# Performance work log

Hardware: AMD Instinct MI355X
Metric: run time of the kernel (lower is better)

Reference implementation:

```python
import jax, jax.numpy as jnp
import numpy as np
from jax import lax

NEG = -1e30  # safe stand-in for -inf in float32
BLANK = 0


def _ctc_loss(log_probs, targets, logits_lengths, targets_lengths):
    # log_probs: (B, T, V) log-softmax over V; targets: (B, S) with labels in [1, V)
    B, T, V = log_probs.shape
    S = targets.shape[1]
    L = 2 * S + 1

    # extended target sequence with interleaved blanks: [b, t0, b, t1, ..., b]
    ext = jnp.full((B, L), BLANK, dtype=targets.dtype)
    ext = ext.at[:, 1::2].set(targets)

    # skip transition (s-2 -> s) allowed iff ext[s] != blank and ext[s] != ext[s-2]
    shifted2 = jnp.concatenate([jnp.full((B, 2), -1, dtype=ext.dtype), ext[:, :-2]], axis=1)
    skip = (ext != BLANK) & (ext != shifted2)  # (B, L)

    # gather per-time log-probs of extended labels: (B, T, L) -> scan axis first (T, B, L)
    lp_ext = jnp.take_along_axis(log_probs, ext[:, None, :], axis=2)
    xs = jnp.moveaxis(lp_ext, 1, 0)

    alpha0 = jnp.where(jnp.arange(L) == 0, 0.0, NEG).astype(log_probs.dtype)
    alpha0 = jnp.broadcast_to(alpha0, (B, L))

    def step(alpha, inputs):
        lp_t, t = inputs
        a2 = jnp.pad(alpha[:, :-1], ((0, 0), (1, 0)), constant_values=NEG)
        a3 = jnp.pad(alpha[:, :-2], ((0, 0), (2, 0)), constant_values=NEG)
        a3 = jnp.where(skip, a3, NEG)
        new = jnp.logaddexp(jnp.logaddexp(alpha, a2), a3) + lp_t
        # freeze alpha past each sequence's length
        alpha = jnp.where((t < logits_lengths)[:, None], new, alpha)
        return alpha, None

    alpha, _ = lax.scan(step, alpha0, (xs, jnp.arange(T)))

    # final states: last label (2*len-1) and trailing blank (2*len)
    e1 = (2 * targets_lengths - 1)[:, None]
    e2 = (2 * targets_lengths)[:, None]
    l1 = jnp.take_along_axis(alpha, e1, axis=1)[:, 0]
    l2 = jnp.take_along_axis(alpha, e2, axis=1)[:, 0]
    return -jnp.logaddexp(l1, l2)  # (B,)


def setup_inputs() -> dict:
    key = jax.random.key(0)
    k1, k2, k3, k4 = jax.random.split(key, 4)
    B, T, V, S = 64, 2000, 256, 200
    logits = jax.random.normal(k1, (B, T, V), dtype=jnp.float32)
    targets = jax.random.randint(k2, (B, S), 1, V)  # avoid blank=0
    logits_lengths = jax.random.randint(k3, (B,), 1500, T + 1)
    targets_lengths = jax.random.randint(k4, (B,), 150, S + 1)
    return {"logits": logits, "targets": targets,
            "logits_lengths": logits_lengths, "targets_lengths": targets_lengths}


def reference(logits, targets, logits_lengths, targets_lengths):
    # after_logsoftmax=False, time_major=False, reduce=None -> per-sample loss (B,)
    log_probs = jax.nn.log_softmax(logits, axis=2)
    return _ctc_loss(log_probs, targets, logits_lengths, targets_lengths)
```

## Files before the change

### kernel.cpp

```cpp
#include <hip/hip_runtime.h>
#include <hip/hip_bf16.h>
#include <cstdint>

#define NEG  (-1e30f)
#define VSZ  256
#define TCAP 2048
#define LN2F 0.6931471805599453f

static __device__ __forceinline__ float    uifu(unsigned u) { return __uint_as_float(u); }
static __device__ __forceinline__ unsigned f2bf(float f) {
    unsigned u = __float_as_uint(f);
    return (u + 0x7fffu + ((u >> 16) & 1u)) >> 16;
}

static __device__ __forceinline__ unsigned pkbf(float lo, float hi) {
    unsigned r;
    asm("v_cvt_pk_bf16_f32 %0, %1, %2" : "=v"(r) : "v"(lo), "v"(hi));
    return r;
}

static __device__ __forceinline__ float wave_sum_dpp(float v) {
    v += __int_as_float(__builtin_amdgcn_update_dpp(0, __float_as_int(v), 0x111, 0xf, 0xf, true));
    v += __int_as_float(__builtin_amdgcn_update_dpp(0, __float_as_int(v), 0x112, 0xf, 0xf, true));
    v += __int_as_float(__builtin_amdgcn_update_dpp(0, __float_as_int(v), 0x114, 0xf, 0xf, true));
    v += __int_as_float(__builtin_amdgcn_update_dpp(0, __float_as_int(v), 0x118, 0xf, 0xf, true));
    v += __int_as_float(__builtin_amdgcn_update_dpp(0, __float_as_int(v), 0x142, 0xa, 0xf, true));
    v += __int_as_float(__builtin_amdgcn_update_dpp(0, __float_as_int(v), 0x143, 0xc, 0xf, true));
    return __int_as_float(__builtin_amdgcn_readlane(__float_as_int(v), 63));
}

__global__ __launch_bounds__(256) void prep7(const float* __restrict__ logits,
                                             const int* __restrict__ targets,
                                             unsigned short* __restrict__ po,
                                             float* __restrict__ pbf,
                                             int T, int S) {
    const int b    = blockIdx.y;
    const int lane = threadIdx.x & 63;
    const int wv   = threadIdx.x >> 6;
    const int rt   = blockIdx.x * 4 + wv;
    if (rt >= T) return;
    const size_t row = (size_t)b * T + rt;
    __shared__ float ldse[4][VSZ];

    const float4* p = (const float4*)(logits + row * VSZ);
    float4 x = p[lane];
    float4 e;
    e.x = __expf(x.x); e.y = __expf(x.y); e.z = __expf(x.z); e.w = __expf(x.w);
    ((float4*)&ldse[wv][0])[lane] = e;

    float s  = (e.x + e.y) + (e.z + e.w);
    float tot = wave_sum_dpp(s);
    float rs  = __builtin_amdgcn_rcpf(tot);

    const int* tg = targets + (size_t)b * S;
    const int c0 = 4 * lane;
    uint2 st;
    if ((S & 3) == 0) {
        int4 tgv = *(const int4*)(tg + min(c0, S - 4));
        float g0 = ldse[wv][tgv.x] * rs;
        float g1 = ldse[wv][tgv.y] * rs;
        float g2 = ldse[wv][tgv.z] * rs;
        float g3 = ldse[wv][tgv.w] * rs;
        st.x = pkbf(g0, g1);
        st.y = pkbf(g2, g3);
    } else {
        float g0 = 0.f, g1 = 0.f, g2 = 0.f, g3 = 0.f;
        if (c0     < S) g0 = ldse[wv][tg[c0]]     * rs;
        if (c0 + 1 < S) g1 = ldse[wv][tg[c0 + 1]] * rs;
        if (c0 + 2 < S) g2 = ldse[wv][tg[c0 + 2]] * rs;
        if (c0 + 3 < S) g3 = ldse[wv][tg[c0 + 3]] * rs;
        st.x = pkbf(g0, g1);
        st.y = pkbf(g2, g3);
    }
    ((uint2*)(po + row * VSZ))[lane] = st;
    if (lane == 0) pbf[row] = e.x * rs;
}

typedef __attribute__((address_space(1))) unsigned int g1u_t;
typedef __attribute__((address_space(3))) unsigned int l3u_t;

static __device__ __forceinline__ void dma16(const void* g, void* l) {
    __builtin_amdgcn_global_load_lds((g1u_t*)(uintptr_t)g,
                                     (l3u_t*)(unsigned int)(uintptr_t)l, 16, 0, 0);
}
static __device__ __forceinline__ void dma4(const void* g, void* l) {
    __builtin_amdgcn_global_load_lds((g1u_t*)(uintptr_t)g,
                                     (l3u_t*)(unsigned int)(uintptr_t)l, 4, 0, 0);
}
static __device__ __forceinline__ float dpp_shr1_f(float v) {
    return __int_as_float(__builtin_amdgcn_update_dpp(0, __float_as_int(v), 0x138, 0xf, 0xf, true));
}
static __device__ __forceinline__ float dpp_shl1_f(float v) {
    return __int_as_float(__builtin_amdgcn_update_dpp(0, __float_as_int(v), 0x130, 0xf, 0xf, true));
}
static __device__ __forceinline__ int dpp_shr1_i(int v) {
    return __builtin_amdgcn_update_dpp(0, v, 0x138, 0xf, 0xf, true);
}
static __device__ __forceinline__ int dpp_shl1_i(int v) {
    return __builtin_amdgcn_update_dpp(0, v, 0x130, 0xf, 0xf, true);
}

template<int W>
static __device__ __forceinline__ void scan_dir(const unsigned short* __restrict__ po_b,
                                                const float* __restrict__ pbr,
                                                unsigned short* __restrict__ d0,
                                                unsigned short* __restrict__ d1,
                                                float* __restrict__ p0,
                                                float* __restrict__ p1,
                                                int lenD, int lm1, int i,
                                                float m1, float m3, float m5, float m7, float n7,
                                                float A[8], int& E) {
    const int  lhalf = i & 31;
    const bool hi    = (i >= 32);
    float dscale = 1.f;

    uint2 ra0, ra1, ra2, ra3, ra4, ra5, ra6, ra7;
    uint2 rb0, rb1, rb2, rb3, rb4, rb5, rb6, rb7;
    float4 qaA, qaB, qbA, qbB;

#define ROWOF(t_) (W ? max(lm1 - (t_), 0) : min((t_), lm1))

#define BODY(XV, PBV) { \
    float pA = uifu(XV.x << 16); \
    float pB = uifu(XV.x & 0xffff0000u); \
    float pC = uifu(XV.y << 16); \
    float pD = uifu(XV.y & 0xffff0000u); \
    if (W == 0) { \
        float hs = dpp_shr1_f(A[7]) * dscale; \
        float s7 = fmaf(m7, A[5], A[6]) + A[7]; \
        float s5 = fmaf(m5, A[3], A[4]) + A[5]; \
        float s3 = fmaf(m3, A[1], A[2]) + A[3]; \
        float s1 = fmaf(m1, hs,   A[0]) + A[1]; \
        A[7] = s7 * pD;  A[6] = (A[6] + A[5]) * (PBV); \
        A[5] = s5 * pC;  A[4] = (A[4] + A[3]) * (PBV); \
        A[3] = s3 * pB;  A[2] = (A[2] + A[1]) * (PBV); \
        A[1] = s1 * pA;  A[0] = (A[0] + hs)   * (PBV); \
    } else { \
        float q0 = A[0] * (PBV), q1 = A[1] * pA; \
        float q2 = A[2] * (PBV), q3 = A[3] * pB; \
        float q4 = A[4] * (PBV), q5 = A[5] * pC; \
        float q6 = A[6] * (PBV), q7 = A[7] * pD; \
        float nq0 = dpp_shl1_f(q0) * dscale; \
        float nq1 = dpp_shl1_f(q1) * dscale; \
        A[0] = q0 + q1; \
        A[1] = fmaf(m3, q3, q1 + q2); \
        A[2] = q2 + q3; \
        A[3] = fmaf(m5, q5, q3 + q4); \
        A[4] = q4 + q5; \
        A[5] = fmaf(m7, q7, q5 + q6); \
        A[6] = q6 + q7; \
        A[7] = fmaf(n7, nq1, q7 + nq0); \
    } \
}

#define RENORM { \
    float lmx = fmaxf(fmaxf(fmaxf(A[0], A[1]), fmaxf(A[2], A[3])), \
                      fmaxf(fmaxf(A[4], A[5]), fmaxf(A[6], A[7]))); \
    unsigned mb = __float_as_uint(lmx) >> 23; \
    mb = mb > 253u ? 253u : mb; \
    float sc_ = uifu((254u - mb) << 23); \
    A[0] *= sc_; A[1] *= sc_; A[2] *= sc_; A[3] *= sc_; \
    A[4] *= sc_; A[5] *= sc_; A[6] *= sc_; A[7] *= sc_; \
    E += (int)mb - 127; \
    int he = W ? dpp_shl1_i(E) : dpp_shr1_i(E); \
    int d  = min(max(he - E, -100), 100); \
    dscale = uifu((unsigned)(d + 127) << 23); \
}

#define STAGE(DN, PN_, TBASE) { \
    _Pragma("unroll") \
    for (int u = 0; u < 32; u += 2) { \
        const int rA = ROWOF((TBASE) + u), rB = ROWOF((TBASE) + u + 1); \
        dma16(po_b + (size_t)(hi ? rB : rA) * VSZ + 8 * lhalf, (DN) + (size_t)u * VSZ); \
    } \
    dma4(pbr + ROWOF((TBASE) + lhalf), (PN_)); \
}

#define LDB(R, QA, QB, DC, PC, BASE) { \
    R##0 = *(const uint2*)((DC) + (size_t)((BASE) + 0) * VSZ + 4 * i); \
    R##1 = *(const uint2*)((DC) + (size_t)((BASE) + 1) * VSZ + 4 * i); \
    R##2 = *(const uint2*)((DC) + (size_t)((BASE) + 2) * VSZ + 4 * i); \
    R##3 = *(const uint2*)((DC) + (size_t)((BASE) + 3) * VSZ + 4 * i); \
    R##4 = *(const uint2*)((DC) + (size_t)((BASE) + 4) * VSZ + 4 * i); \
    R##5 = *(const uint2*)((DC) + (size_t)((BASE) + 5) * VSZ + 4 * i); \
    R##6 = *(const uint2*)((DC) + (size_t)((BASE) + 6) * VSZ + 4 * i); \
    R##7 = *(const uint2*)((DC) + (size_t)((BASE) + 7) * VSZ + 4 * i); \
    QA = *(const float4*)((PC) + (BASE)); \
    QB = *(const float4*)((PC) + (BASE) + 4); \
}

#define CMP8(R, QA, QB) { \
    BODY(R##0, QA.x) BODY(R##1, QA.y) BODY(R##2, QA.z) BODY(R##3, QA.w) RENORM \
    BODY(R##4, QB.x) BODY(R##5, QB.y) BODY(R##6, QB.z) BODY(R##7, QB.w) RENORM \
}

#define SBAR __builtin_amdgcn_sched_barrier(0)

#define SUPERF(DC, PC, DN, PN_) { \
    STAGE(DN, PN_, t0 + 32) \
    asm volatile("s_waitcnt vmcnt(17)" ::: "memory"); \
    LDB(ra, qaA, qaB, DC, PC, 0) \
    SBAR; \
    LDB(rb, qbA, qbB, DC, PC, 8) \
    SBAR; \
    CMP8(ra, qaA, qaB) \
    LDB(ra, qaA, qaB, DC, PC, 16) \
    SBAR; \
    CMP8(rb, qbA, qbB) \
    LDB(rb, qbA, qbB, DC, PC, 24) \
    SBAR; \
    CMP8(ra, qaA, qaB) \
    CMP8(rb, qbA, qbB) \
}

    STAGE(d0, p0, 0)

    int t0 = 0;
    const int nfull = lenD >> 5;
    const int ntail = lenD & 31;
    unsigned short* cur = d0; unsigned short* nxt = d1;
    float* pc = p0;  float* pn = p1;

    #pragma clang loop unroll(disable)
    for (int sl = 0; sl < nfull; ++sl) {
        SUPERF(cur, pc, nxt, pn)
        t0 += 32;
        unsigned short* td = cur; cur = nxt; nxt = td;
        float* tp = pc; pc = pn; pn = tp;
    }
    if (ntail) {
        asm volatile("s_waitcnt vmcnt(0)" ::: "memory");
        #pragma clang loop unroll(disable)
        for (int u = 0; u < ntail; ++u) {
            uint2 x = *(const uint2*)(cur + (size_t)u * VSZ + 4 * i);
            float pb = pc[u];
            BODY(x, pb)
            if ((u & 3) == 3) RENORM
        }
    }
#undef SUPERF
#undef SBAR
#undef CMP8
#undef LDB
#undef STAGE
#undef RENORM
#undef BODY
#undef ROWOF
}

__global__ __launch_bounds__(128, 1) void ctc_scan12(const unsigned short* __restrict__ po,
                                                     const float* __restrict__ pbf,
                                                     const int* __restrict__ targets,
                                                     const int* __restrict__ llen_p,
                                                     const int* __restrict__ tlen_p,
                                                     float* __restrict__ out,
                                                     int T, int S) {
    const int b   = blockIdx.x;
    const int w   = threadIdx.x >> 6;
    const int i   = threadIdx.x & 63;
    const int len  = llen_p[b];
    const int lm1  = len - 1;
    const int lenF = (len + 1) >> 1;
    const int lenD = w ? (len - lenF) : lenF;

    __shared__ __align__(16) unsigned short dF0[32 * VSZ], dF1[32 * VSZ];
    __shared__ __align__(16) unsigned short dB0[32 * VSZ], dB1[32 * VSZ];
    __shared__ __align__(16) float pF0[64], pF1[64], pB0[64], pB1[64];
    __shared__ __align__(16) float bfin[512];
    __shared__ int bein[64];

    const int* tg  = targets + (size_t)b * S;
    const int Sm1  = S - 1;
    const int j0   = 4 * i;
    const int tm   = tg[max(min(j0 - 1, Sm1), 0)];
    const int t0l  = tg[min(j0,     Sm1)];
    const int t1l  = tg[min(j0 + 1, Sm1)];
    const int t2l  = tg[min(j0 + 2, Sm1)];
    const int t3l  = tg[min(j0 + 3, Sm1)];
    const int t4l  = tg[min(j0 + 4, Sm1)];
    const float m1 = (j0 == 0 || t0l != tm) ? 1.f : 0.f;
    const float m3 = (t1l != t0l) ? 1.f : 0.f;
    const float m5 = (t2l != t1l) ? 1.f : 0.f;
    const float m7 = (t3l != t2l) ? 1.f : 0.f;
    const float n7 = (t4l != t3l) ? 1.f : 0.f;

    const unsigned short* po_b = po + (size_t)b * T * VSZ;
    const float*          pbr  = pbf + (size_t)b * T;

    float A[8];
    int   E = 0;
    if (w == 0) {
        #pragma unroll
        for (int k = 0; k < 8; ++k) A[k] = 0.f;
        if (i == 0) A[0] = 1.f;
        scan_dir<0>(po_b, pbr, dF0, dF1, pF0, pF1,
                    lenD, lm1, i, m1, m3, m5, m7, n7, A, E);
    } else {
        const int tl = tlen_p[b];
        const int s1 = 2 * tl - 1, s2 = 2 * tl;
        #pragma unroll
        for (int k = 0; k < 8; ++k)
            A[k] = (8 * i + k == s1 || 8 * i + k == s2) ? 1.f : 0.f;
        scan_dir<1>(po_b, pbr, dB0, dB1, pB0, pB1,
                    lenD, lm1, i, m1, m3, m5, m7, n7, A, E);
        *(float4*)&bfin[8 * i]     = make_float4(A[0], A[1], A[2], A[3]);
        *(float4*)&bfin[8 * i + 4] = make_float4(A[4], A[5], A[6], A[7]);
        bein[i] = E;
    }
    __syncthreads();
    if (w == 0) {
        float4 u0 = *(float4*)&bfin[8 * i];
        float4 u1 = *(float4*)&bfin[8 * i + 4];
        float dsum = A[0]*u0.x + A[1]*u0.y + A[2]*u0.z + A[3]*u0.w
                   + A[4]*u1.x + A[5]*u1.y + A[6]*u1.z + A[7]*u1.w;
        float li = (dsum > 0.f) ? __logf(dsum) + (float)(E + bein[i]) * LN2F : NEG;
        float mx = li;
        #pragma unroll
        for (int off = 32; off; off >>= 1) mx = fmaxf(mx, __shfl_xor(mx, off, 64));
        float ss = __expf(li - mx);
        #pragma unroll
        for (int off = 32; off; off >>= 1) ss += __shfl_xor(ss, off, 64);
        if (i == 0) out[b] = -(mx + __logf(ss));
    }
}

__device__ __forceinline__ void barrier_lgkm() {
    __asm__ volatile("s_waitcnt lgkmcnt(0)\n\ts_barrier" ::: "memory");
}

__global__ __launch_bounds__(256) void lse_kernel(const float* __restrict__ logits,
                                                  float* __restrict__ lse,
                                                  int nrows) {
    int row = blockIdx.x * 4 + (threadIdx.x >> 6);
    if (row >= nrows) return;
    int lane = threadIdx.x & 63;
    const float4* p = (const float4*)(logits + (size_t)row * VSZ);
    float4 x = p[lane];
    float m = fmaxf(fmaxf(x.x, x.y), fmaxf(x.z, x.w));
    #pragma unroll
    for (int off = 32; off; off >>= 1) m = fmaxf(m, __shfl_xor(m, off, 64));
    float s = __expf(x.x - m) + __expf(x.y - m) + __expf(x.z - m) + __expf(x.w - m);
    #pragma unroll
    for (int off = 32; off; off >>= 1) s += __shfl_xor(s, off, 64);
    if (lane == 0) lse[row] = m + __logf(s);
}

__device__ __forceinline__ float lae(float a, float b) {
    float mx = fmaxf(a, b);
    float mn = fminf(a, b);
    return mx + __logf(1.0f + __expf(mn - mx));
}

__global__ __launch_bounds__(256, 1) void ctc_scan_fb(const float* __restrict__ logits,
                                                      const int* __restrict__ targets,
                                                      const int* __restrict__ llen_p,
                                                      const int* __restrict__ tlen_p,
                                                      const float* __restrict__ lse,
                                                      float* __restrict__ out,
                                                      int T, int S) {
    const int b = blockIdx.x;
    const int i = threadIdx.x;
    const int len = llen_p[b];

    __shared__ float blankv[TCAP];
    __shared__ float abuf[2][256 + 2];
    __shared__ float wsum[4];

    const float* __restrict__ lgb  = logits + (size_t)b * T * VSZ;
    const float* __restrict__ lseb = lse + (size_t)b * T;

    int  lab  = 0;
    bool skip = false;
    if (i < S) {
        lab = targets[b * S + i];
        int prev = (i >= 1) ? targets[b * S + i - 1] : -1;
        skip = (lab != prev);
    }
    for (int t = i; t < len; t += 256) blankv[t] = lgb[(size_t)t * VSZ];
    if (i < 2) abuf[i][0] = NEG;
    __syncthreads();

    float aEven = (i == 0) ? 0.0f : NEG;
    float aOdd  = NEG;
    const int lm1 = len - 1;
    float v0 = lgb[(size_t)lab];
    float v1 = lgb[(size_t)min(1, lm1) * VSZ + lab];
    float v2 = lgb[(size_t)min(2, lm1) * VSZ + lab];

    for (int t = 0; t < len; ++t) {
        float v3 = lgb[(size_t)min(t + 3, lm1) * VSZ + lab];
        float blv = blankv[t];
        abuf[t & 1][i + 1] = aOdd;
        barrier_lgkm();
        float nb = abuf[t & 1][i];
        float ne = lae(aEven, nb) + blv;
        float no = lae(lae(aOdd, aEven), skip ? nb : NEG) + v0;
        aEven = ne; aOdd = no;
        v0 = v1; v1 = v2; v2 = v3;
    }

    blankv[2 * i]     = aEven;
    blankv[2 * i + 1] = aOdd;
    float part = 0.f;
    for (int t = i; t < len; t += 256) part += lseb[t];
    #pragma unroll
    for (int off = 32; off; off >>= 1) part += __shfl_xor(part, off, 64);
    if ((i & 63) == 0) wsum[i >> 6] = part;
    __syncthreads();
    if (i == 0) {
        int tl = tlen_p[b];
        float s = wsum[0] + wsum[1] + wsum[2] + wsum[3];
        out[b] = s - lae(blankv[2 * tl - 1], blankv[2 * tl]);
    }
}

extern "C" void kernel_launch(void* const* d_in, const int* in_sizes, int n_in,
                              void* d_out, int out_size, void* d_ws, size_t ws_size,
                              hipStream_t stream) {
    const float* logits  = (const float*)d_in[0];
    const int*   targets = (const int*)d_in[1];
    const int*   llen    = (const int*)d_in[2];
    const int*   tlen    = (const int*)d_in[3];
    float*       out     = (float*)d_out;

    const int B = in_sizes[2];
    const int S = in_sizes[1] / B;
    const int T = in_sizes[0] / (B * VSZ);
    const int nrows = B * T;

    const size_t need = (size_t)nrows * VSZ * sizeof(unsigned short)
                      + (size_t)nrows * sizeof(float);
    if (ws_size >= need) {
        unsigned short* po = (unsigned short*)d_ws;
        float* pbf = (float*)(po + (size_t)nrows * VSZ);
        dim3 grid((T + 3) / 4, B);
        prep7<<<grid, 256, 0, stream>>>(logits, targets, po, pbf, T, S);
        ctc_scan12<<<B, 128, 0, stream>>>(po, pbf, targets, llen, tlen, out, T, S);
    } else {
        float* lse = (float*)d_ws;
        lse_kernel<<<(nrows + 3) / 4, 256, 0, stream>>>(logits, lse, nrows);
        ctc_scan_fb<<<B, 256, 0, stream>>>(logits, targets, llen, tlen, lse, out, T, S);
    }
}
```

Before: 263.6 us.

## Split global-to-LDS staging into dedicated producer waves with barrier handoff

```diff
diff --git a/kernel.cpp b/kernel.cpp
--- a/kernel.cpp
+++ b/kernel.cpp
@@ -100,25 +100,43 @@
     return __builtin_amdgcn_update_dpp(0, v, 0x130, 0xf, 0xf, true);
 }
 
+#define ROWOF(t_) (W ? max(lm1 - (t_), 0) : min((t_), lm1))
+
 template<int W>
-static __device__ __forceinline__ void scan_dir(const unsigned short* __restrict__ po_b,
-                                                const float* __restrict__ pbr,
-                                                unsigned short* __restrict__ d0,
-                                                unsigned short* __restrict__ d1,
-                                                float* __restrict__ p0,
-                                                float* __restrict__ p1,
-                                                int lenD, int lm1, int i,
-                                                float m1, float m3, float m5, float m7, float n7,
-                                                float A[8], int& E) {
+static __device__ __forceinline__ void stage_dir(const unsigned short* __restrict__ po_b,
+                                                 const float* __restrict__ pbr,
+                                                 unsigned short* __restrict__ d0,
+                                                 unsigned short* __restrict__ d1,
+                                                 float* __restrict__ p0,
+                                                 float* __restrict__ p1,
+                                                 int lenD, int lm1, int i, int nwinMax) {
     const int  lhalf = i & 31;
     const bool hi    = (i >= 32);
-    float dscale = 1.f;
-
-    uint2 ra0, ra1, ra2, ra3, ra4, ra5, ra6, ra7;
-    uint2 rb0, rb1, rb2, rb3, rb4, rb5, rb6, rb7;
-    float4 qaA, qaB, qbA, qbB;
-
-#define ROWOF(t_) (W ? max(lm1 - (t_), 0) : min((t_), lm1))
+    const int  nwin  = (lenD + 31) >> 5;
+
+#define STAGE(DN, PN_, TBASE) { \
+    _Pragma("unroll") \
+    for (int u = 0; u < 32; u += 2) { \
+        const int rA = ROWOF((TBASE) + u), rB = ROWOF((TBASE) + u + 1); \
+        dma16(po_b + (size_t)(hi ? rB : rA) * VSZ + 8 * lhalf, (DN) + (size_t)u * VSZ); \
+    } \
+    dma4(pbr + ROWOF((TBASE) + lhalf), (PN_)); \
+}
+
+    STAGE(d0, p0, 0)
+    asm volatile("s_waitcnt vmcnt(0)" ::: "memory");
+    #pragma clang loop unroll(disable)
+    for (int k = 0; k < nwinMax; ++k) {
+        __syncthreads();
+        if (k + 1 < nwin) {
+            unsigned short* DN = ((k + 1) & 1) ? d1 : d0;
+            float*          PN = ((k + 1) & 1) ? p1 : p0;
+            STAGE(DN, PN, 32 * (k + 1))
+            asm volatile("s_waitcnt vmcnt(0)" ::: "memory");
+        }
+    }
+#undef STAGE
+}
 
 #define BODY(XV, PBV) { \
     float pA = uifu(XV.x << 16); \
@@ -167,15 +185,6 @@
     dscale = uifu((unsigned)(d + 127) << 23); \
 }
 
-#define STAGE(DN, PN_, TBASE) { \
-    _Pragma("unroll") \
-    for (int u = 0; u < 32; u += 2) { \
-        const int rA = ROWOF((TBASE) + u), rB = ROWOF((TBASE) + u + 1); \
-        dma16(po_b + (size_t)(hi ? rB : rA) * VSZ + 8 * lhalf, (DN) + (size_t)u * VSZ); \
-    } \
-    dma4(pbr + ROWOF((TBASE) + lhalf), (PN_)); \
-}
-
 #define LDB(R, QA, QB, DC, PC, BASE) { \
     R##0 = *(const uint2*)((DC) + (size_t)((BASE) + 0) * VSZ + 4 * i); \
     R##1 = *(const uint2*)((DC) + (size_t)((BASE) + 1) * VSZ + 4 * i); \
@@ -196,59 +205,59 @@
 
 #define SBAR __builtin_amdgcn_sched_barrier(0)
 
-#define SUPERF(DC, PC, DN, PN_) { \
-    STAGE(DN, PN_, t0 + 32) \
-    asm volatile("s_waitcnt vmcnt(17)" ::: "memory"); \
-    LDB(ra, qaA, qaB, DC, PC, 0) \
-    SBAR; \
-    LDB(rb, qbA, qbB, DC, PC, 8) \
-    SBAR; \
-    CMP8(ra, qaA, qaB) \
-    LDB(ra, qaA, qaB, DC, PC, 16) \
-    SBAR; \
-    CMP8(rb, qbA, qbB) \
-    LDB(rb, qbA, qbB, DC, PC, 24) \
-    SBAR; \
-    CMP8(ra, qaA, qaB) \
-    CMP8(rb, qbA, qbB) \
-}
-
-    STAGE(d0, p0, 0)
-
-    int t0 = 0;
+template<int W>
+static __device__ __forceinline__ void scan_dir(const unsigned short* __restrict__ d0,
+                                                const unsigned short* __restrict__ d1,
+                                                const float* __restrict__ p0,
+                                                const float* __restrict__ p1,
+                                                int lenD, int i,
+                                                float m1, float m3, float m5, float m7, float n7,
+                                                float A[8], int& E, int nwinMax) {
+    float dscale = 1.f;
+    uint2 ra0, ra1, ra2, ra3, ra4, ra5, ra6, ra7;
+    uint2 rb0, rb1, rb2, rb3, rb4, rb5, rb6, rb7;
+    float4 qaA, qaB, qbA, qbB;
     const int nfull = lenD >> 5;
     const int ntail = lenD & 31;
-    unsigned short* cur = d0; unsigned short* nxt = d1;
-    float* pc = p0;  float* pn = p1;
 
     #pragma clang loop unroll(disable)
-    for (int sl = 0; sl < nfull; ++sl) {
-        SUPERF(cur, pc, nxt, pn)
-        t0 += 32;
-        unsigned short* td = cur; cur = nxt; nxt = td;
-        float* tp = pc; pc = pn; pn = tp;
-    }
-    if (ntail) {
-        asm volatile("s_waitcnt vmcnt(0)" ::: "memory");
-        #pragma clang loop unroll(disable)
-        for (int u = 0; u < ntail; ++u) {
-            uint2 x = *(const uint2*)(cur + (size_t)u * VSZ + 4 * i);
-            float pb = pc[u];
-            BODY(x, pb)
-            if ((u & 3) == 3) RENORM
+    for (int k = 0; k < nwinMax; ++k) {
+        __syncthreads();
+        const unsigned short* DC = (k & 1) ? d1 : d0;
+        const float*          PC = (k & 1) ? p1 : p0;
+        if (k < nfull) {
+            LDB(ra, qaA, qaB, DC, PC, 0)
+            SBAR;
+            LDB(rb, qbA, qbB, DC, PC, 8)
+            SBAR;
+            CMP8(ra, qaA, qaB)
+            LDB(ra, qaA, qaB, DC, PC, 16)
+            SBAR;
+            CMP8(rb, qbA, qbB)
+            LDB(rb, qbA, qbB, DC, PC, 24)
+            SBAR;
+            CMP8(ra, qaA, qaB)
+            CMP8(rb, qbA, qbB)
+        } else if (k == nfull && ntail) {
+            #pragma clang loop unroll(disable)
+            for (int u = 0; u < ntail; ++u) {
+                uint2 x = *(const uint2*)(DC + (size_t)u * VSZ + 4 * i);
+                float pb = PC[u];
+                BODY(x, pb)
+                if ((u & 3) == 3) RENORM
+            }
         }
     }
-#undef SUPERF
+}
+
 #undef SBAR
 #undef CMP8
 #undef LDB
-#undef STAGE
 #undef RENORM
 #undef BODY
 #undef ROWOF
-}
-
-__global__ __launch_bounds__(128, 1) void ctc_scan12(const unsigned short* __restrict__ po,
+
+__global__ __launch_bounds__(256, 1) void ctc_scan14(const unsigned short* __restrict__ po,
                                                      const float* __restrict__ pbf,
                                                      const int* __restrict__ targets,
                                                      const int* __restrict__ llen_p,
@@ -261,7 +270,10 @@
     const int len  = llen_p[b];
     const int lm1  = len - 1;
     const int lenF = (len + 1) >> 1;
-    const int lenD = w ? (len - lenF) : lenF;
+    const int lenB = len - lenF;
+    const int nwinF = (lenF + 31) >> 5;
+    const int nwinB = (lenB + 31) >> 5;
+    const int nwinMax = nwinF > nwinB ? nwinF : nwinB;
 
     __shared__ __align__(16) unsigned short dF0[32 * VSZ], dF1[32 * VSZ];
     __shared__ __align__(16) unsigned short dB0[32 * VSZ], dB1[32 * VSZ];
@@ -269,40 +281,50 @@
     __shared__ __align__(16) float bfin[512];
     __shared__ int bein[64];
 
-    const int* tg  = targets + (size_t)b * S;
-    const int Sm1  = S - 1;
-    const int j0   = 4 * i;
-    const int tm   = tg[max(min(j0 - 1, Sm1), 0)];
-    const int t0l  = tg[min(j0,     Sm1)];
-    const int t1l  = tg[min(j0 + 1, Sm1)];
-    const int t2l  = tg[min(j0 + 2, Sm1)];
-    const int t3l  = tg[min(j0 + 3, Sm1)];
-    const int t4l  = tg[min(j0 + 4, Sm1)];
-    const float m1 = (j0 == 0 || t0l != tm) ? 1.f : 0.f;
-    const float m3 = (t1l != t0l) ? 1.f : 0.f;
-    const float m5 = (t2l != t1l) ? 1.f : 0.f;
-    const float m7 = (t3l != t2l) ? 1.f : 0.f;
-    const float n7 = (t4l != t3l) ? 1.f : 0.f;
-
     const unsigned short* po_b = po + (size_t)b * T * VSZ;
     const float*          pbr  = pbf + (size_t)b * T;
 
     float A[8];
     int   E = 0;
-    if (w == 0) {
-        #pragma unroll
-        for (int k = 0; k < 8; ++k) A[k] = 0.f;
-        if (i == 0) A[0] = 1.f;
-        scan_dir<0>(po_b, pbr, dF0, dF1, pF0, pF1,
-                    lenD, lm1, i, m1, m3, m5, m7, n7, A, E);
+
+    if (w < 2) {
+        const int* tg  = targets + (size_t)b * S;
+        const int Sm1  = S - 1;
+        const int j0   = 4 * i;
+        const int tm   = tg[max(min(j0 - 1, Sm1), 0)];
+        const int t0l  = tg[min(j0,     Sm1)];
+        const int t1l  = tg[min(j0 + 1, Sm1)];
+        const int t2l  = tg[min(j0 + 2, Sm1)];
+        const int t3l  = tg[min(j0 + 3, Sm1)];
+        const int t4l  = tg[min(j0 + 4, Sm1)];
+        const float m1 = (j0 == 0 || t0l != tm) ? 1.f : 0.f;
+        const float m3 = (t1l != t0l) ? 1.f : 0.f;
+        const float m5 = (t2l != t1l) ? 1.f : 0.f;
+        const float m7 = (t3l != t2l) ? 1.f : 0.f;
+        const float n7 = (t4l != t3l) ? 1.f : 0.f;
+
+        if (w == 0) {
+            #pragma unroll
+            for (int k = 0; k < 8; ++k) A[k] = 0.f;
+            if (i == 0) A[0] = 1.f;
+            scan_dir<0>(dF0, dF1, pF0, pF1, lenF, i,
+                        m1, m3, m5, m7, n7, A, E, nwinMax);
+        } else {
+            const int tl = tlen_p[b];
+            const int s1 = 2 * tl - 1, s2 = 2 * tl;
+            #pragma unroll
+            for (int k = 0; k < 8; ++k)
+                A[k] = (8 * i + k == s1 || 8 * i + k == s2) ? 1.f : 0.f;
+            scan_dir<1>(dB0, dB1, pB0, pB1, lenB, i,
+                        m1, m3, m5, m7, n7, A, E, nwinMax);
+        }
+    } else if (w == 2) {
+        stage_dir<0>(po_b, pbr, dF0, dF1, pF0, pF1, lenF, lm1, i, nwinMax);
     } else {
-        const int tl = tlen_p[b];
-        const int s1 = 2 * tl - 1, s2 = 2 * tl;
-        #pragma unroll
-        for (int k = 0; k < 8; ++k)
-            A[k] = (8 * i + k == s1 || 8 * i + k == s2) ? 1.f : 0.f;
-        scan_dir<1>(po_b, pbr, dB0, dB1, pB0, pB1,
-                    lenD, lm1, i, m1, m3, m5, m7, n7, A, E);
+        stage_dir<1>(po_b, pbr, dB0, dB1, pB0, pB1, lenB, lm1, i, nwinMax);
+    }
+
+    if (w == 1) {
         *(float4*)&bfin[8 * i]     = make_float4(A[0], A[1], A[2], A[3]);
         *(float4*)&bfin[8 * i + 4] = make_float4(A[4], A[5], A[6], A[7]);
         bein[i] = E;
@@ -435,7 +457,7 @@
         float* pbf = (float*)(po + (size_t)nrows * VSZ);
         dim3 grid((T + 3) / 4, B);
         prep7<<<grid, 256, 0, stream>>>(logits, targets, po, pbf, T, S);
-        ctc_scan12<<<B, 128, 0, stream>>>(po, pbf, targets, llen, tlen, out, T, S);
+        ctc_scan14<<<B, 256, 0, stream>>>(po, pbf, targets, llen, tlen, out, T, S);
     } else {
         float* lse = (float*)d_ws;
         lse_kernel<<<(nrows + 3) / 4, 256, 0, stream>>>(logits, lse, nrows);
```

Result: slower. 269.7 us (+2.3%).
